# Optimization experiments

Hardware: AMD Instinct MI355X
Metric: run time of the kernel (lower is better)

The kernel has to match this reference:

```python
import jax, jax.numpy as jnp
import numpy as np

DECAY = 0.99
EPS = 1e-5
BETA = 0.25

def _l2norm(v, axis=-1):
    # F.normalize: x / max(||x||, 1e-12)
    n = jnp.sqrt(jnp.sum(v * v, axis=axis, keepdims=True))
    return v / jnp.maximum(n, 1e-12)

def setup_inputs() -> dict:
    key = jax.random.key(0)
    k0, k1, k2, k3 = jax.random.split(key, 4)
    B, C, H, W, E, K = 8, 256, 64, 64, 32, 8192
    x = jax.random.normal(k0, (B, C, H, W), jnp.float32)
    Wq = jax.random.normal(k1, (E, C), jnp.float32) * 0.05  # 1x1 conv kernel
    bq = jnp.zeros((E,), jnp.float32)
    emb = jax.random.normal(k2, (K, E), jnp.float32)
    emb = _l2norm(emb, axis=1)  # matches F.normalize init in __init__
    ema_cluster_size = jnp.ones((K,), jnp.float32)
    ema_weight = emb  # consistent post-init EMA state
    return {"x": x, "Wq": Wq, "bq": bq, "embedding": emb,
            "ema_cluster_size": ema_cluster_size, "ema_weight": ema_weight}

def reference(x, Wq, bq, embedding, ema_cluster_size, ema_weight):
    B, C, H, W = x.shape
    E = Wq.shape[0]
    K = embedding.shape[0]
    # quant_conv: 1x1 conv == per-pixel linear
    z = jnp.einsum('bchw,ec->behw', x, Wq) + bq[None, :, None, None]  # [B,E,H,W]
    z_flat = z.transpose(0, 2, 3, 1).reshape(-1, E)  # [N,E]
    # get_idx(use_znorm=True): cosine similarity argmax (== argmin L2 on normalized)
    zn = _l2norm(z_flat, axis=1)
    en = _l2norm(embedding, axis=1)
    indices = jnp.argmax(zn @ en.T, axis=1)  # [N]
    # codebook gather (raw embedding, as in torch)
    z_q = embedding[indices].reshape(B, H, W, E).transpose(0, 3, 1, 2)  # [B,E,H,W]
    # EMA update (training path; scatter == one-hot.T @ z_flat / one-hot.sum)
    counts = jax.ops.segment_sum(jnp.ones((z_flat.shape[0],), z_flat.dtype), indices, num_segments=K)
    dw = jax.ops.segment_sum(z_flat, indices, num_segments=K)  # [K,E]
    new_cs = DECAY * ema_cluster_size + (1.0 - DECAY) * counts
    new_w = DECAY * ema_weight + (1.0 - DECAY) * dw
    n = jnp.sum(new_cs)
    cs_smoothed = (new_cs + EPS) / (n + K * EPS) * n
    new_embedding = new_w / cs_smoothed[:, None]
    # commitment loss + straight-through
    qloss = BETA * jnp.mean((jax.lax.stop_gradient(z_q) - z) ** 2)
    z_q_st = z + jax.lax.stop_gradient(z_q - z)
    return (z_q_st, indices.reshape(B, H, W), qloss, new_embedding, new_cs, new_w)
```

## Files before the change

kernel.cpp:

```cpp
#include <hip/hip_runtime.h>

#define B_ 8
#define C_ 256
#define HW_ 4096
#define E_ 32
#define K_ 8192
#define N_ 32768
#define NCHUNK 8
#define KC_ (K_ / NCHUNK)
#define NSTAGE (KC_ / 128)
#define KSEG 16
#define PIX 128

#define DECAY_ 0.99f
#define OMD_   0.01f
#define EPS_   1e-5f
#define BETA_  0.25f

#define O_ZQ   0
#define O_IDX  1048576
#define O_QL   1081344
#define O_NEMB 1081345
#define O_NCS  1343489
#define O_NW   1351681

#define WS_EH   0u
#define WS_EM   131072u
#define WS_Z    262144u
#define WS_PACK 1310720u
#define WS_PCS  1835008u
#define WS_QP   1835024u

typedef float f32x4 __attribute__((ext_vector_type(4)));
typedef short s16x8 __attribute__((ext_vector_type(8)));
typedef unsigned long long u64;

__device__ __forceinline__ unsigned short f2bf(float f) {
    unsigned u = __float_as_uint(f);
    u = u + 0x7fffu + ((u >> 16) & 1u);
    return (unsigned short)(u >> 16);
}
__device__ __forceinline__ float bf2f(unsigned short h) {
    return __uint_as_float(((unsigned)h) << 16);
}
__device__ __forceinline__ unsigned ford(float f) {
    unsigned u = __float_as_uint(f);
    return (u & 0x80000000u) ? ~u : (u | 0x80000000u);
}
__device__ __forceinline__ int imax(int a, int b) { return a > b ? a : b; }
__device__ __forceinline__ int imin(int a, int b) { return a < b ? a : b; }

__device__ __forceinline__ void gload_lds16(const void* g, void* l) {
    __builtin_amdgcn_global_load_lds(
        (const __attribute__((address_space(1))) unsigned int*)g,
        (__attribute__((address_space(3))) unsigned int*)l, 16, 0, 0);
}

__global__ __launch_bounds__(512) void k_pre(const float* __restrict__ emb,
                                             const float* __restrict__ cs,
                                             uint4* __restrict__ eh16,
                                             uint4* __restrict__ em16,
                                             float* __restrict__ part_cs,
                                             const float* __restrict__ x,
                                             const float* __restrict__ Wq,
                                             const float* __restrict__ bq,
                                             float* __restrict__ zout) {
    __shared__ float wqt[C_ * E_];
    __shared__ float red8[8];
    int tid = threadIdx.x;

    if (blockIdx.x < 16) {
        int k = blockIdx.x * 512 + tid;
        const float4* r = (const float4*)(emb + (size_t)k * E_);
        float v[E_];
        float ss = 0.f;
#pragma unroll
        for (int i = 0; i < 8; i++) {
            float4 t = r[i];
            v[i*4+0] = t.x; v[i*4+1] = t.y; v[i*4+2] = t.z; v[i*4+3] = t.w;
            ss += t.x*t.x + t.y*t.y + t.z*t.z + t.w*t.w;
        }
        float inv = 1.0f / fmaxf(sqrtf(ss), 1e-12f);
        unsigned short h1a[E_], h2a[E_];
#pragma unroll
        for (int e = 0; e < E_; e++) {
            float en = v[e] * inv;
            unsigned short h1 = f2bf(en);
            float r1 = en - bf2f(h1);
            h1a[e] = h1; h2a[e] = f2bf(r1);
        }
        int t = k >> 4, c15 = k & 15;
#pragma unroll
        for (int i = 0; i < 4; i++) {
            eh16[t * 64 + i * 16 + c15] = ((uint4*)h1a)[i];
            em16[t * 64 + i * 16 + c15] = ((uint4*)h2a)[i];
        }

        float cv = cs[blockIdx.x * 512 + tid];
#pragma unroll
        for (int off = 32; off > 0; off >>= 1) cv += __shfl_down(cv, off);
        int lane = tid & 63, wid = tid >> 6;
        if (lane == 0) red8[wid] = cv;
        __syncthreads();
        if (tid == 0) {
            float s = 0.f;
#pragma unroll
            for (int i = 0; i < 8; i++) s += red8[i];
            part_cs[blockIdx.x] = s;
        }
        return;
    }

    int zb = blockIdx.x - 16;
#pragma unroll
    for (int i = 0; i < 16; i++) {
        int g = i * 512 + tid;
        int e = g >> 8;
        int c = g & 255;
        wqt[c * E_ + e] = Wq[g];
    }
    __syncthreads();
    int lp = tid & 63, eg = tid >> 6;
    int n0 = zb * 64 + lp;
    int b  = n0 >> 12, hw = n0 & (HW_ - 1);
    const float* xp = x + (size_t)b * C_ * HW_ + hw;
    float a0 = 0.f, a1 = 0.f, a2 = 0.f, a3 = 0.f;
#pragma unroll 8
    for (int c = 0; c < C_; c++) {
        float xv = xp[(size_t)c * HW_];
        float4 wv = *(const float4*)(wqt + c * E_ + eg * 4);
        a0 += xv * wv.x; a1 += xv * wv.y; a2 += xv * wv.z; a3 += xv * wv.w;
    }
    *(float4*)(zout + (size_t)n0 * E_ + eg * 4) =
        make_float4(a0 + bq[eg*4+0], a1 + bq[eg*4+1],
                    a2 + bq[eg*4+2], a3 + bq[eg*4+3]);
}

__global__ __launch_bounds__(512) void k_score_mfma(const float* __restrict__ zws,
                                                    const char* __restrict__ ehb,
                                                    const char* __restrict__ emb_b,
                                                    int2* __restrict__ pk2) {
    __shared__ __align__(16) char smem[32768];

    int tid  = threadIdx.x;
    int lane = tid & 63;
    int w    = tid >> 6;
    int chunk = blockIdx.y;

    s16x8 a1, a2;
    {
        int ploc = w * 16 + (lane & 15);
        int n0   = blockIdx.x * PIX + ploc;
        int e0   = (lane >> 4) * 8;
        const float4* zp = (const float4*)(zws + (size_t)n0 * E_ + e0);
        float4 z0 = zp[0], z1 = zp[1];
        float zz[8] = {z0.x, z0.y, z0.z, z0.w, z1.x, z1.y, z1.z, z1.w};
#pragma unroll
        for (int j = 0; j < 8; j++) {
            float zv = zz[j] * 134217728.0f;
            unsigned short h1 = f2bf(zv);
            float r1 = zv - bf2f(h1);
            a1[j] = (short)h1; a2[j] = (short)f2bf(r1);
        }
    }

    const char* srcp[2];
#pragma unroll
    for (int i = 0; i < 2; i++) {
        int d = i * 512 + tid;
        int pl = d >> 9, dd = d & 511;
        srcp[i] = (pl ? emb_b : ehb) + (size_t)chunk * (KC_ * 64) + dd * 16;
    }

#pragma unroll
    for (int i = 0; i < 2; i++)
        gload_lds16(srcp[i], smem + (i * 512 + tid) * 16);
    __syncthreads();

    int rbase = 8191 - chunk * KC_ - (lane & 15);
    int bq1[4], bq2[4];
#pragma unroll
    for (int j = 0; j < 4; j++) { bq1[j] = (int)0x80000000; bq2[j] = (int)0x80000000; }
    f32x4 zero4 = {0.f, 0.f, 0.f, 0.f};

    for (int st = 0; st < NSTAGE; st++) {
        if (st + 1 < NSTAGE) {
            char* dst = smem + ((st + 1) & 1) * 16384;
#pragma unroll
            for (int i = 0; i < 2; i++)
                gload_lds16(srcp[i] + (size_t)(st + 1) * 8192, dst + (i * 512 + tid) * 16);
        }
        const char* cur = smem + (st & 1) * 16384;
        int rst = rbase - st * 128;

#pragma unroll
        for (int g = 0; g < 2; g++) {
            int ct = g * 4;
            s16x8 b1[4], b2[4];
#pragma unroll
            for (int q = 0; q < 4; q++) {
                b1[q] = ((const s16x8*)(cur +        (ct + q) * 1024))[lane];
                b2[q] = ((const s16x8*)(cur + 8192 + (ct + q) * 1024))[lane];
            }
            f32x4 acc[4];
#pragma unroll
            for (int q = 0; q < 4; q++)
                acc[q] = __builtin_amdgcn_mfma_f32_16x16x32_bf16(a1, b1[q], zero4, 0, 0, 0);
#pragma unroll
            for (int q = 0; q < 4; q++)
                acc[q] = __builtin_amdgcn_mfma_f32_16x16x32_bf16(a1, b2[q], acc[q], 0, 0, 0);
#pragma unroll
            for (int q = 0; q < 4; q++)
                acc[q] = __builtin_amdgcn_mfma_f32_16x16x32_bf16(a2, b1[q], acc[q], 0, 0, 0);
            int r0 = rst - ct * 16;
#pragma unroll
            for (int j = 0; j < 4; j++) {
                int v0 = ((int)acc[0][j] & (int)0xFFFFE000) | r0;
                int v1 = ((int)acc[1][j] & (int)0xFFFFE000) | (r0 - 16);
                int v2 = ((int)acc[2][j] & (int)0xFFFFE000) | (r0 - 32);
                int v3 = ((int)acc[3][j] & (int)0xFFFFE000) | (r0 - 48);
                int hi = imax(imax(v0, v1), imax(v2, v3));
                int m  = imin(bq1[j], hi);
                bq1[j] = imax(bq1[j], hi);
                bq2[j] = imax(bq2[j], m);
            }
        }
        __syncthreads();
    }

#pragma unroll
    for (int off = 1; off < 16; off <<= 1) {
#pragma unroll
        for (int j = 0; j < 4; j++) {
            int o1 = __shfl_xor(bq1[j], off, 64);
            int o2 = __shfl_xor(bq2[j], off, 64);
            int m  = imin(bq1[j], o1);
            bq1[j] = imax(bq1[j], o1);
            bq2[j] = imax(imax(bq2[j], o2), m);
        }
    }
    if ((lane & 15) == 0) {
        int rowbase = blockIdx.x * PIX + w * 16 + (lane >> 4) * 4;
#pragma unroll
        for (int j = 0; j < 4; j++)
            pk2[(size_t)chunk * N_ + rowbase + j] = make_int2(bq1[j], bq2[j]);
    }
}

__device__ __forceinline__ float rescore(const float* __restrict__ emb, int k,
                                         const float* zrow) {
    const float4* r = (const float4*)(emb + (size_t)k * E_);
    float4 v[8];
    float ss = 0.f;
#pragma unroll
    for (int i = 0; i < 8; i++) {
        v[i] = r[i];
        ss += v[i].x * v[i].x + v[i].y * v[i].y + v[i].z * v[i].z + v[i].w * v[i].w;
    }
    float inv = 1.0f / fmaxf(sqrtf(ss), 1e-12f);
    const float4* zp = (const float4*)zrow;
    float sx = 0.f, sy = 0.f, sz = 0.f, sw = 0.f;
#pragma unroll
    for (int i = 0; i < 8; i++) {
        float4 e4 = make_float4(v[i].x * inv, v[i].y * inv, v[i].z * inv, v[i].w * inv);
        float4 zr = zp[i];
        sx += zr.x * e4.x; sy += zr.y * e4.y;
        sz += zr.z * e4.z; sw += zr.w * e4.w;
    }
    return (sx + sy) + (sz + sw);
}

__global__ __launch_bounds__(256) void k_scatter(const float* __restrict__ zws,
                                                 const int2* __restrict__ pk2,
                                                 const float* __restrict__ emb,
                                                 float* __restrict__ out_zq,
                                                 float* __restrict__ out_idx,
                                                 float* __restrict__ qpart) {
    __shared__ float zbuf[32 * E_];
    __shared__ int   idxs_s[32];
    __shared__ float red[4];
    int tid = threadIdx.x;

    const float4* zsrc = (const float4*)(zws + (size_t)blockIdx.x * 32 * E_);
    ((float4*)zbuf)[tid] = zsrc[tid];
    __syncthreads();

    {
        int p = tid >> 3, c8 = tid & 7;
        int nn = blockIdx.x * 32 + p;
        int2 c2 = pk2[(size_t)c8 * N_ + nn];
        u64 pkd = 0;
#pragma unroll
        for (int t = 0; t < 2; t++) {
            int raw = t ? c2.y : c2.x;
            int k = 8191 - (raw & 0x1fff);
            k = k < 0 ? 0 : (k > K_ - 1 ? K_ - 1 : k);
            float s = rescore(emb, k, zbuf + p * E_);
            u64 pk = ((u64)ford(s) << 32) | (unsigned)(K_ - 1 - k);
            pkd = pkd > pk ? pkd : pk;
        }
        u64 o = __shfl_xor(pkd, 1, 64); pkd = pkd > o ? pkd : o;
        o = __shfl_xor(pkd, 2, 64);     pkd = pkd > o ? pkd : o;
        o = __shfl_xor(pkd, 4, 64);     pkd = pkd > o ? pkd : o;
        if (c8 == 0) {
            int bi = K_ - 1 - (int)(unsigned)(pkd & 0xffffffffu);
            idxs_s[p] = bi;
            out_idx[nn] = (float)bi;
        }
    }
    __syncthreads();

    int lp = tid & 31, eg = tid >> 5;
    int n  = blockIdx.x * 32 + lp;
    int b  = n >> 12, hw = n & (HW_ - 1);
    int idx = idxs_s[lp];
    float4 e4 = *(const float4*)(emb + (size_t)idx * E_ + eg * 4);
    float* o = out_zq + (size_t)b * E_ * HW_ + (size_t)(eg * 4) * HW_ + hw;

    float z0 = zbuf[lp * E_ + eg * 4 + 0];
    float z1 = zbuf[lp * E_ + eg * 4 + 1];
    float z2 = zbuf[lp * E_ + eg * 4 + 2];
    float z3 = zbuf[lp * E_ + eg * 4 + 3];
    o[0]                 = e4.x;
    o[(size_t)1 * HW_]   = e4.y;
    o[(size_t)2 * HW_]   = e4.z;
    o[(size_t)3 * HW_]   = e4.w;
    float d0 = e4.x - z0, d1 = e4.y - z1, d2 = e4.z - z2, d3 = e4.w - z3;
    float sq = d0*d0 + d1*d1 + d2*d2 + d3*d3;

#pragma unroll
    for (int off = 32; off > 0; off >>= 1) sq += __shfl_down(sq, off);
    int lane = tid & 63, wid = tid >> 6;
    if (lane == 0) red[wid] = sq;
    __syncthreads();
    if (tid == 0) qpart[blockIdx.x] = red[0] + red[1] + red[2] + red[3];
}

__global__ __launch_bounds__(256) void k_dwfinal(const float* __restrict__ zws,
                                                 const float* __restrict__ idxf,
                                                 const float* __restrict__ cs,
                                                 const float* __restrict__ ew,
                                                 const float* __restrict__ part_cs,
                                                 const float* __restrict__ qpart,
                                                 float* __restrict__ out_nw,
                                                 float* __restrict__ out_nemb,
                                                 float* __restrict__ out_ncs,
                                                 float* __restrict__ out_ql) {
    __shared__ float acc[KSEG * E_];
    __shared__ int   cnt_s[KSEG];
    __shared__ int   plist[2048];
    __shared__ int   lcnt;
    __shared__ float nsum_s;
    int tid = threadIdx.x;
    int kbase = blockIdx.x * KSEG;

#pragma unroll
    for (int i = 0; i < KSEG * E_ / 256; i++) acc[tid + i * 256] = 0.f;
    if (tid < KSEG) cnt_s[tid] = 0;
    if (tid == 0) lcnt = 0;
    __syncthreads();

    const float4* idx4 = (const float4*)idxf;
    for (int tile = 0; tile < N_ / 2048; ++tile) {
        int pbase = tile * 2048 + tid * 8;
        float4 f0 = idx4[tile * 512 + tid * 2];
        float4 f1 = idx4[tile * 512 + tid * 2 + 1];
        float fs[8] = {f0.x, f0.y, f0.z, f0.w, f1.x, f1.y, f1.z, f1.w};
#pragma unroll
        for (int s = 0; s < 8; s++) {
            unsigned d = (unsigned)((int)fs[s] - kbase);
            if (d < (unsigned)KSEG) {
                int pos = atomicAdd(&lcnt, 1);
                plist[pos] = ((pbase + s) << 5) | (int)d;
                atomicAdd(cnt_s + (int)d, 1);
            }
        }
        __syncthreads();
        int cnt = lcnt;
        int e = tid & 31;
        for (int m = tid >> 5; m < cnt; m += 8) {
            int pk = plist[m];
            int nn = pk >> 5;
            float zv = zws[(size_t)nn * E_ + e];
            atomicAdd(acc + (pk & 31) * E_ + e, zv);
        }
        __syncthreads();
        if (tid == 0) lcnt = 0;
        __syncthreads();
    }

    if (tid < 64) {
        float s = (tid < 16) ? part_cs[tid] : 0.f;
        s += __shfl_down(s, 8);
        s += __shfl_down(s, 4);
        s += __shfl_down(s, 2);
        s += __shfl_down(s, 1);
        if (tid == 0) nsum_s = DECAY_ * s + OMD_ * (float)N_;
    }
    __syncthreads();
    float nsum = nsum_s;

#pragma unroll
    for (int i = 0; i < KSEG * E_ / 256; i++) {
        int local = tid + i * 256;
        int kl = local >> 5, c = local & 31;
        int k = kbase + kl;
        float v = DECAY_ * ew[(size_t)k * E_ + c] + OMD_ * acc[local];
        out_nw[(size_t)k * E_ + c] = v;
        float csk = DECAY_ * cs[k] + OMD_ * (float)cnt_s[kl];
        float denom = (csk + EPS_) / (nsum + (float)K_ * EPS_) * nsum;
        out_nemb[(size_t)k * E_ + c] = v / denom;
        if (c == 0) out_ncs[k] = csk;
    }

    if (blockIdx.x == 0 && tid < 64) {
        float s = 0.f;
#pragma unroll
        for (int i = 0; i < 16; i++) s += qpart[tid + i * 64];
#pragma unroll
        for (int off = 32; off > 0; off >>= 1) s += __shfl_down(s, off);
        if (tid == 0) out_ql[0] = BETA_ * s / (float)(B_ * E_ * HW_);
    }
}

extern "C" void kernel_launch(void* const* d_in, const int* in_sizes, int n_in,
                              void* d_out, int out_size, void* d_ws, size_t ws_size,
                              hipStream_t stream) {
    const float* x   = (const float*)d_in[0];
    const float* Wq  = (const float*)d_in[1];
    const float* bq  = (const float*)d_in[2];
    const float* emb = (const float*)d_in[3];
    const float* cs  = (const float*)d_in[4];
    const float* ew  = (const float*)d_in[5];
    float* out = (float*)d_out;
    float* ws  = (float*)d_ws;

    k_pre<<<16 + N_ / 64, 512, 0, stream>>>(emb, cs,
        (uint4*)(ws + WS_EH), (uint4*)(ws + WS_EM), ws + WS_PCS,
        x, Wq, bq, ws + WS_Z);
    k_score_mfma<<<dim3(N_ / PIX, NCHUNK), 512, 0, stream>>>(ws + WS_Z,
        (const char*)(ws + WS_EH), (const char*)(ws + WS_EM),
        (int2*)(ws + WS_PACK));
    k_scatter<<<N_ / 32, 256, 0, stream>>>(ws + WS_Z,
        (const int2*)(ws + WS_PACK), emb,
        out + O_ZQ, out + O_IDX, ws + WS_QP);
    k_dwfinal<<<K_ / KSEG, 256, 0, stream>>>(ws + WS_Z, out + O_IDX, cs, ew,
                                             ws + WS_PCS, ws + WS_QP,
                                             out + O_NW, out + O_NEMB,
                                             out + O_NCS, out + O_QL);
}
```

Before: 191.4 us.

## Process two pixel tiles per wave to reuse codebook LDS fragments

```diff
diff --git a/kernel.cpp b/kernel.cpp
--- a/kernel.cpp
+++ b/kernel.cpp
@@ -10,7 +10,7 @@
 #define KC_ (K_ / NCHUNK)
 #define NSTAGE (KC_ / 128)
 #define KSEG 16
-#define PIX 128
+#define PIX 256
 
 #define DECAY_ 0.99f
 #define OMD_   0.01f
@@ -147,20 +147,26 @@
     int w    = tid >> 6;
     int chunk = blockIdx.y;
 
-    s16x8 a1, a2;
+    s16x8 a1A, a2A, a1B, a2B;
     {
-        int ploc = w * 16 + (lane & 15);
-        int n0   = blockIdx.x * PIX + ploc;
-        int e0   = (lane >> 4) * 8;
-        const float4* zp = (const float4*)(zws + (size_t)n0 * E_ + e0);
-        float4 z0 = zp[0], z1 = zp[1];
-        float zz[8] = {z0.x, z0.y, z0.z, z0.w, z1.x, z1.y, z1.z, z1.w};
-#pragma unroll
-        for (int j = 0; j < 8; j++) {
-            float zv = zz[j] * 134217728.0f;
-            unsigned short h1 = f2bf(zv);
-            float r1 = zv - bf2f(h1);
-            a1[j] = (short)h1; a2[j] = (short)f2bf(r1);
+        int plocA = w * 32 + (lane & 15);
+        int e0    = (lane >> 4) * 8;
+#pragma unroll
+        for (int s = 0; s < 2; s++) {
+            int n0 = blockIdx.x * PIX + plocA + s * 16;
+            const float4* zp = (const float4*)(zws + (size_t)n0 * E_ + e0);
+            float4 z0 = zp[0], z1 = zp[1];
+            float zz[8] = {z0.x, z0.y, z0.z, z0.w, z1.x, z1.y, z1.z, z1.w};
+            s16x8 h1v, h2v;
+#pragma unroll
+            for (int j = 0; j < 8; j++) {
+                float zv = zz[j] * 134217728.0f;
+                unsigned short h1 = f2bf(zv);
+                float r1 = zv - bf2f(h1);
+                h1v[j] = (short)h1; h2v[j] = (short)f2bf(r1);
+            }
+            if (s == 0) { a1A = h1v; a2A = h2v; }
+            else        { a1B = h1v; a2B = h2v; }
         }
     }
 
@@ -178,9 +184,12 @@
     __syncthreads();
 
     int rbase = 8191 - chunk * KC_ - (lane & 15);
-    int bq1[4], bq2[4];
-#pragma unroll
-    for (int j = 0; j < 4; j++) { bq1[j] = (int)0x80000000; bq2[j] = (int)0x80000000; }
+    int bqA1[4], bqA2[4], bqB1[4], bqB2[4];
+#pragma unroll
+    for (int j = 0; j < 4; j++) {
+        bqA1[j] = (int)0x80000000; bqA2[j] = (int)0x80000000;
+        bqB1[j] = (int)0x80000000; bqB2[j] = (int)0x80000000;
+    }
     f32x4 zero4 = {0.f, 0.f, 0.f, 0.f};
 
     for (int st = 0; st < NSTAGE; st++) {
@@ -202,28 +211,53 @@
                 b1[q] = ((const s16x8*)(cur +        (ct + q) * 1024))[lane];
                 b2[q] = ((const s16x8*)(cur + 8192 + (ct + q) * 1024))[lane];
             }
-            f32x4 acc[4];
-#pragma unroll
-            for (int q = 0; q < 4; q++)
-                acc[q] = __builtin_amdgcn_mfma_f32_16x16x32_bf16(a1, b1[q], zero4, 0, 0, 0);
-#pragma unroll
-            for (int q = 0; q < 4; q++)
-                acc[q] = __builtin_amdgcn_mfma_f32_16x16x32_bf16(a1, b2[q], acc[q], 0, 0, 0);
-#pragma unroll
-            for (int q = 0; q < 4; q++)
-                acc[q] = __builtin_amdgcn_mfma_f32_16x16x32_bf16(a2, b1[q], acc[q], 0, 0, 0);
             int r0 = rst - ct * 16;
-#pragma unroll
-            for (int j = 0; j < 4; j++) {
-                int v0 = ((int)acc[0][j] & (int)0xFFFFE000) | r0;
-                int v1 = ((int)acc[1][j] & (int)0xFFFFE000) | (r0 - 16);
-                int v2 = ((int)acc[2][j] & (int)0xFFFFE000) | (r0 - 32);
-                int v3 = ((int)acc[3][j] & (int)0xFFFFE000) | (r0 - 48);
-                int hi = imax(imax(v0, v1), imax(v2, v3));
-                int m  = imin(bq1[j], hi);
-                bq1[j] = imax(bq1[j], hi);
-                bq2[j] = imax(bq2[j], m);
+            {
+                f32x4 acc[4];
+#pragma unroll
+                for (int q = 0; q < 4; q++)
+                    acc[q] = __builtin_amdgcn_mfma_f32_16x16x32_bf16(a1A, b1[q], zero4, 0, 0, 0);
+#pragma unroll
+                for (int q = 0; q < 4; q++)
+                    acc[q] = __builtin_amdgcn_mfma_f32_16x16x32_bf16(a1A, b2[q], acc[q], 0, 0, 0);
+#pragma unroll
+                for (int q = 0; q < 4; q++)
+                    acc[q] = __builtin_amdgcn_mfma_f32_16x16x32_bf16(a2A, b1[q], acc[q], 0, 0, 0);
+#pragma unroll
+                for (int j = 0; j < 4; j++) {
+                    int v0 = ((int)acc[0][j] & (int)0xFFFFE000) | r0;
+                    int v1 = ((int)acc[1][j] & (int)0xFFFFE000) | (r0 - 16);
+                    int v2 = ((int)acc[2][j] & (int)0xFFFFE000) | (r0 - 32);
+                    int v3 = ((int)acc[3][j] & (int)0xFFFFE000) | (r0 - 48);
+                    int hi = imax(imax(v0, v1), imax(v2, v3));
+                    int m  = imin(bqA1[j], hi);
+                    bqA1[j] = imax(bqA1[j], hi);
+                    bqA2[j] = imax(bqA2[j], m);
+                }
             }
+            {
+                f32x4 acc[4];
+#pragma unroll
+                for (int q = 0; q < 4; q++)
+                    acc[q] = __builtin_amdgcn_mfma_f32_16x16x32_bf16(a1B, b1[q], zero4, 0, 0, 0);
+#pragma unroll
+                for (int q = 0; q < 4; q++)
+                    acc[q] = __builtin_amdgcn_mfma_f32_16x16x32_bf16(a1B, b2[q], acc[q], 0, 0, 0);
+#pragma unroll
+                for (int q = 0; q < 4; q++)
+                    acc[q] = __builtin_amdgcn_mfma_f32_16x16x32_bf16(a2B, b1[q], acc[q], 0, 0, 0);
+#pragma unroll
+                for (int j = 0; j < 4; j++) {
+                    int v0 = ((int)acc[0][j] & (int)0xFFFFE000) | r0;
+                    int v1 = ((int)acc[1][j] & (int)0xFFFFE000) | (r0 - 16);
+                    int v2 = ((int)acc[2][j] & (int)0xFFFFE000) | (r0 - 32);
+                    int v3 = ((int)acc[3][j] & (int)0xFFFFE000) | (r0 - 48);
+                    int hi = imax(imax(v0, v1), imax(v2, v3));
+                    int m  = imin(bqB1[j], hi);
+                    bqB1[j] = imax(bqB1[j], hi);
+                    bqB2[j] = imax(bqB2[j], m);
+                }
+            }
         }
         __syncthreads();
     }
@@ -232,18 +266,25 @@
     for (int off = 1; off < 16; off <<= 1) {
 #pragma unroll
         for (int j = 0; j < 4; j++) {
-            int o1 = __shfl_xor(bq1[j], off, 64);
-            int o2 = __shfl_xor(bq2[j], off, 64);
-            int m  = imin(bq1[j], o1);
-            bq1[j] = imax(bq1[j], o1);
-            bq2[j] = imax(imax(bq2[j], o2), m);
+            int o1 = __shfl_xor(bqA1[j], off, 64);
+            int o2 = __shfl_xor(bqA2[j], off, 64);
+            int m  = imin(bqA1[j], o1);
+            bqA1[j] = imax(bqA1[j], o1);
+            bqA2[j] = imax(imax(bqA2[j], o2), m);
+            int p1 = __shfl_xor(bqB1[j], off, 64);
+            int p2 = __shfl_xor(bqB2[j], off, 64);
+            int n  = imin(bqB1[j], p1);
+            bqB1[j] = imax(bqB1[j], p1);
+            bqB2[j] = imax(imax(bqB2[j], p2), n);
         }
     }
     if ((lane & 15) == 0) {
-        int rowbase = blockIdx.x * PIX + w * 16 + (lane >> 4) * 4;
-#pragma unroll
-        for (int j = 0; j < 4; j++)
-            pk2[(size_t)chunk * N_ + rowbase + j] = make_int2(bq1[j], bq2[j]);
+        int rowbase = blockIdx.x * PIX + w * 32 + (lane >> 4) * 4;
+#pragma unroll
+        for (int j = 0; j < 4; j++) {
+            pk2[(size_t)chunk * N_ + rowbase + j]      = make_int2(bqA1[j], bqA2[j]);
+            pk2[(size_t)chunk * N_ + rowbase + 16 + j] = make_int2(bqB1[j], bqB2[j]);
+        }
     }
 }
 
```

After: 188.1 us. About the same (-1.7%).
